# Performance work log

Measured on AMD Instinct MI355X. Metric: run time of the kernel, lower is better.

Reference implementation:

```python
import jax, jax.numpy as jnp
import numpy as np

N_GENES = 20000   # num_all_genes
D = 256           # embedding_dim
NNZ = 640000      # nonzeros in GO adjacency (~32 avg degree)
N_COND = 2000     # number of conditions
B = 16384         # batch size
MAXG = 5          # max_genes_per_condition
L = 2             # num_gnn_layers


def setup_inputs() -> dict:
    key = jax.random.key(0)
    ks = jax.random.split(key, 12)
    cond_idx = jax.random.randint(ks[0], (B,), 0, N_COND, dtype=jnp.int32)
    pert_embedding = jax.random.normal(ks[1], (N_GENES, D), jnp.float32) * 0.05
    gnn_kernels = jax.random.normal(ks[2], (L, D, D), jnp.float32) * 0.05
    mlp_w1 = jax.random.normal(ks[3], (D, D), jnp.float32) * 0.05
    mlp_b1 = jnp.zeros((D,), jnp.float32)
    mlp_w2 = jax.random.normal(ks[4], (D, D), jnp.float32) * 0.05
    mlp_b2 = jnp.zeros((D,), jnp.float32)
    adj_row = jax.random.randint(ks[5], (NNZ,), 0, N_GENES, dtype=jnp.int64)
    adj_col = jax.random.randint(ks[6], (NNZ,), 0, N_GENES, dtype=jnp.int64)
    adj_vals = jax.random.uniform(ks[7], (NNZ,), jnp.float32)
    cond_gene_idx = jax.random.randint(ks[8], (N_COND, MAXG), 0, N_GENES, dtype=jnp.int32)
    counts = jax.random.randint(ks[9], (N_COND,), 0, MAXG + 1)
    cond_gene_mask = (jnp.arange(MAXG)[None, :] < counts[:, None]).astype(jnp.float32)
    # padded slots get -1 index like the original (later clamped to 0)
    cond_gene_idx = jnp.where(cond_gene_mask > 0, cond_gene_idx, -1)
    return {
        'cond_idx': cond_idx,
        'pert_embedding': pert_embedding,
        'gnn_kernels': gnn_kernels,
        'mlp_w1': mlp_w1, 'mlp_b1': mlp_b1,
        'mlp_w2': mlp_w2, 'mlp_b2': mlp_b2,
        'adj_row': adj_row, 'adj_col': adj_col, 'adj_vals': adj_vals,
        'cond_gene_idx': cond_gene_idx, 'cond_gene_mask': cond_gene_mask,
    }


def reference(cond_idx, pert_embedding, gnn_kernels, mlp_w1, mlp_b1,
              mlp_w2, mlp_b2, adj_row, adj_col, adj_vals,
              cond_gene_idx, cond_gene_mask):
    # --- GNN over the full gene graph (sparse adjacency @ dense emb, then dense kernel) ---
    emb = pert_embedding  # [N, D]
    for i in range(L):
        # SpMM: aggregated[r] = sum_{nnz with row r} vals * emb[col]
        msgs = adj_vals[:, None] * emb[adj_col]            # [NNZ, D]
        agg = jax.ops.segment_sum(msgs, adj_row, num_segments=N_GENES)  # [N, D]
        emb = agg @ gnn_kernels[i]                          # [N, D]
        if i < L - 1:
            emb = jax.nn.relu(emb)

    # --- per-condition gather of up to MAXG gene embeddings, masked sum ---
    gidx = cond_gene_idx[cond_idx]          # [B, MAXG] int
    gmask = cond_gene_mask[cond_idx]        # [B, MAXG]
    gidx_safe = jnp.maximum(gidx, 0)
    gene_embs = emb[gidx_safe]              # [B, MAXG, D]
    summed = jnp.sum(gene_embs * gmask[:, :, None], axis=1)  # [B, D]
    n_genes = jnp.sum(gmask, axis=1)        # [B]

    # --- small MLP (applied when n_genes > 1), identity when ==1, zeros when ==0 ---
    h = jax.nn.relu(summed @ mlp_w1 + mlp_b1)
    mlp_out = jax.nn.relu(h @ mlp_w2 + mlp_b2)  # [B, D]

    n = n_genes[:, None]
    out = jnp.where(n == 0.0, 0.0, jnp.where(n == 1.0, summed, mlp_out))
    return out
```

## Files before the change

### kernel.cpp

```cpp
#include <hip/hip_runtime.h>

static constexpr int N_GENES = 20000;
static constexpr int D       = 256;
static constexpr int NNZ     = 640000;
static constexpr int BATCH   = 16384;
static constexpr int MAXG    = 5;
static constexpr int NR      = 8;
static constexpr int NB      = N_GENES * NR;
static constexpr int SCAN_BLKS = NB / 256;

using bf16x8 = __attribute__((ext_vector_type(8))) short;
using f32x4  = __attribute__((ext_vector_type(4))) float;

__device__ __forceinline__ unsigned short f2bf(float f) {
  unsigned int u = __builtin_bit_cast(unsigned int, f);
  u += 0x7fffu + ((u >> 16) & 1u);
  return (unsigned short)(u >> 16);
}
__device__ __forceinline__ float bf2f(unsigned short h) {
  unsigned int u = ((unsigned int)h) << 16;
  return __builtin_bit_cast(float, u);
}
__device__ __forceinline__ void gload16(const void* g, void* l) {
  __builtin_amdgcn_global_load_lds(
      (const __attribute__((address_space(1))) unsigned int*)g,
      (__attribute__((address_space(3))) unsigned int*)l, 16, 0, 0);
}
__device__ __forceinline__ unsigned colrange(int col) {
  return ((unsigned)col * 26215u) >> 26;
}

__global__ void count_buckets(const int* __restrict__ adj_row,
                              const int* __restrict__ adj_col, int* __restrict__ cnt) {
  int e = blockIdx.x * 256 + threadIdx.x;
  int r = adj_row[e];
  atomicAdd(&cnt[(r << 3) | colrange(adj_col[e])], 1);
}

__global__ __launch_bounds__(256)
void scan_partial(const int* __restrict__ cnt, int* __restrict__ bsum) {
  __shared__ int red[256];
  int b = blockIdx.x, t = threadIdx.x;
  red[t] = cnt[b * 256 + t];
  __syncthreads();
  for (int off = 128; off > 0; off >>= 1) {
    if (t < off) red[t] += red[t + off];
    __syncthreads();
  }
  if (t == 0) bsum[b] = red[0];
}

__global__ __launch_bounds__(1024)
void scan_mid(const int* __restrict__ bsum, int* __restrict__ bpre) {
  __shared__ int s[1024];
  int t = threadIdx.x;
  int x = (t < SCAN_BLKS) ? bsum[t] : 0;
  s[t] = x;
  __syncthreads();
  for (int off = 1; off < 1024; off <<= 1) {
    int v = (t >= off) ? s[t - off] : 0;
    __syncthreads();
    s[t] += v;
    __syncthreads();
  }
  if (t < SCAN_BLKS) bpre[t] = s[t] - x;
}

__global__ __launch_bounds__(256)
void scan_final(const int* __restrict__ cnt, const int* __restrict__ bpre,
                int* __restrict__ bptr, int* __restrict__ fill_ctr) {
  __shared__ int s[256];
  int b = blockIdx.x, t = threadIdx.x, i = b * 256 + t;
  int x = cnt[i];
  s[t] = x;
  __syncthreads();
  for (int off = 1; off < 256; off <<= 1) {
    int v = (t >= off) ? s[t - off] : 0;
    __syncthreads();
    s[t] += v;
    __syncthreads();
  }
  int e = bpre[b] + s[t] - x;
  bptr[i] = e;
  fill_ctr[i] = e;
  if (b == 0 && t == 0) bptr[NB] = NNZ;
}

__global__ __launch_bounds__(256)
void fused_fill_conv(const int* __restrict__ adj_row, const int* __restrict__ adj_col,
                     const float* __restrict__ vals, int* __restrict__ fill_ctr,
                     unsigned int* __restrict__ edges,
                     const float* __restrict__ gk, const float* __restrict__ w1,
                     const float* __restrict__ w2,
                     char* __restrict__ whi, char* __restrict__ wlo,
                     const float* __restrict__ pert, ushort4* __restrict__ pert_bf) {
  int b = blockIdx.x, t = threadIdx.x;
  if (b < 2500) {
    int e = b * 256 + t;
    int r = adj_row[e];
    int col = adj_col[e];
    int p = atomicAdd(&fill_ctr[(r << 3) | colrange(col)], 1);
    edges[p] = (unsigned int)col | ((unsigned int)f2bf(vals[e]) << 16);
  } else if (b < 2628) {
    int g = (b - 2500) * 256 + t;
    int wid = g >> 13, rest = g & 8191;
    const float* W = (wid == 0) ? gk : (wid == 1) ? gk + 65536 : (wid == 2) ? w1 : w2;
    int c  = rest >> 9;
    int nc = c >> 2, kt = c & 3;
    int o  = (rest & 511) << 4;
    int n  = o >> 7;
    int wb = (o & 127) ^ ((n & 7) << 4);
    int k  = wb >> 1;
    size_t obase = ((size_t)wid << 17) + ((size_t)c << 13) + o;
    unsigned short* ph = (unsigned short*)(whi + obase);
    unsigned short* pl = (unsigned short*)(wlo + obase);
    #pragma unroll
    for (int e2 = 0; e2 < 8; ++e2) {
      float f = W[(size_t)(kt * 64 + k + e2) * 256 + nc * 64 + n];
      unsigned short h = f2bf(f);
      ph[e2] = h;
      pl[e2] = f2bf(f - bf2f(h));
    }
  } else {
    int i = (b - 2628) * 256 + t;
    float4 v = reinterpret_cast<const float4*>(pert)[i];
    ushort4 r4;
    r4.x = f2bf(v.x); r4.y = f2bf(v.y); r4.z = f2bf(v.z); r4.w = f2bf(v.w);
    pert_bf[i] = r4;
  }
}

__global__ __launch_bounds__(256)
void spmm_csr_img(const int* __restrict__ bptr, const unsigned int* __restrict__ edges,
                  const unsigned short* __restrict__ src,
                  char* __restrict__ hi_img, char* __restrict__ lo_img) {
  int row = blockIdx.x * 4 + (threadIdx.x >> 6);
  int lane = threadIdx.x & 63;
  int beg = bptr[row << 3], end = bptr[(row << 3) + 8];
  const unsigned short* sp = src + lane * 4;
  float4 acc = {0.f, 0.f, 0.f, 0.f};
  int j = beg;
  for (; j + 8 <= end; j += 8) {
    unsigned int e0 = edges[j],     e1 = edges[j + 1], e2 = edges[j + 2], e3 = edges[j + 3];
    unsigned int e4 = edges[j + 4], e5 = edges[j + 5], e6 = edges[j + 6], e7 = edges[j + 7];
    ushort4 g0 = *reinterpret_cast<const ushort4*>(sp + (size_t)(e0 & 0xFFFFu) * D);
    ushort4 g1 = *reinterpret_cast<const ushort4*>(sp + (size_t)(e1 & 0xFFFFu) * D);
    ushort4 g2 = *reinterpret_cast<const ushort4*>(sp + (size_t)(e2 & 0xFFFFu) * D);
    ushort4 g3 = *reinterpret_cast<const ushort4*>(sp + (size_t)(e3 & 0xFFFFu) * D);
    ushort4 g4 = *reinterpret_cast<const ushort4*>(sp + (size_t)(e4 & 0xFFFFu) * D);
    ushort4 g5 = *reinterpret_cast<const ushort4*>(sp + (size_t)(e5 & 0xFFFFu) * D);
    ushort4 g6 = *reinterpret_cast<const ushort4*>(sp + (size_t)(e6 & 0xFFFFu) * D);
    ushort4 g7 = *reinterpret_cast<const ushort4*>(sp + (size_t)(e7 & 0xFFFFu) * D);
    float v0 = bf2f(e0 >> 16), v1 = bf2f(e1 >> 16), v2 = bf2f(e2 >> 16), v3 = bf2f(e3 >> 16);
    float v4 = bf2f(e4 >> 16), v5 = bf2f(e5 >> 16), v6 = bf2f(e6 >> 16), v7 = bf2f(e7 >> 16);
    acc.x += v0 * bf2f(g0.x); acc.y += v0 * bf2f(g0.y); acc.z += v0 * bf2f(g0.z); acc.w += v0 * bf2f(g0.w);
    acc.x += v1 * bf2f(g1.x); acc.y += v1 * bf2f(g1.y); acc.z += v1 * bf2f(g1.z); acc.w += v1 * bf2f(g1.w);
    acc.x += v2 * bf2f(g2.x); acc.y += v2 * bf2f(g2.y); acc.z += v2 * bf2f(g2.z); acc.w += v2 * bf2f(g2.w);
    acc.x += v3 * bf2f(g3.x); acc.y += v3 * bf2f(g3.y); acc.z += v3 * bf2f(g3.z); acc.w += v3 * bf2f(g3.w);
    acc.x += v4 * bf2f(g4.x); acc.y += v4 * bf2f(g4.y); acc.z += v4 * bf2f(g4.z); acc.w += v4 * bf2f(g4.w);
    acc.x += v5 * bf2f(g5.x); acc.y += v5 * bf2f(g5.y); acc.z += v5 * bf2f(g5.z); acc.w += v5 * bf2f(g5.w);
    acc.x += v6 * bf2f(g6.x); acc.y += v6 * bf2f(g6.y); acc.z += v6 * bf2f(g6.z); acc.w += v6 * bf2f(g6.w);
    acc.x += v7 * bf2f(g7.x); acc.y += v7 * bf2f(g7.y); acc.z += v7 * bf2f(g7.z); acc.w += v7 * bf2f(g7.w);
  }
  for (; j < end; ++j) {
    unsigned int e = edges[j];
    ushort4 g = *reinterpret_cast<const ushort4*>(sp + (size_t)(e & 0xFFFFu) * D);
    float v = bf2f(e >> 16);
    acc.x += v * bf2f(g.x); acc.y += v * bf2f(g.y); acc.z += v * bf2f(g.z); acc.w += v * bf2f(g.w);
  }
  int mt = row >> 7, r = row & 127, kt = lane >> 4;
  int wb = ((lane & 15) << 3) ^ ((r & 7) << 4);
  size_t off = ((size_t)(mt * 4 + kt) << 14) + (size_t)r * 128 + wb;
  float a4[4] = {acc.x, acc.y, acc.z, acc.w};
  ushort4 hi, lo;
  unsigned short* ph = (unsigned short*)&hi;
  unsigned short* pl = (unsigned short*)&lo;
  #pragma unroll
  for (int e = 0; e < 4; ++e) {
    unsigned short h = f2bf(a4[e]);
    ph[e] = h;
    pl[e] = f2bf(a4[e] - bf2f(h));
  }
  *reinterpret_cast<ushort4*>(hi_img + off) = hi;
  *reinterpret_cast<ushort4*>(lo_img + off) = lo;
}

__global__ __launch_bounds__(256)
void gather_conditions(const int* __restrict__ cond_idx, const int* __restrict__ cg_idx,
                       const float* __restrict__ cg_mask, const float* __restrict__ emb,
                       float* __restrict__ out, char* __restrict__ hi_img,
                       char* __restrict__ lo_img, float* __restrict__ ngenes) {
  int b = blockIdx.x * 4 + (threadIdx.x >> 6);
  int lane = threadIdx.x & 63;
  int c = cond_idx[b];
  float4 acc = {0.f, 0.f, 0.f, 0.f};
  float n = 0.f;
  #pragma unroll
  for (int g = 0; g < MAXG; ++g) {
    float m = cg_mask[c * MAXG + g];
    n += m;
    if (m > 0.f) {
      int gi = cg_idx[c * MAXG + g];
      float4 e = *reinterpret_cast<const float4*>(emb + (size_t)gi * D + lane * 4);
      acc.x += m * e.x; acc.y += m * e.y; acc.z += m * e.z; acc.w += m * e.w;
    }
  }
  *reinterpret_cast<float4*>(out + (size_t)b * D + lane * 4) = acc;
  int mt = b >> 7, r = b & 127, kt = lane >> 4;
  int wb = ((lane & 15) << 3) ^ ((r & 7) << 4);
  size_t off = ((size_t)(mt * 4 + kt) << 14) + (size_t)r * 128 + wb;
  float a4[4] = {acc.x, acc.y, acc.z, acc.w};
  ushort4 hi, lo;
  unsigned short* ph = (unsigned short*)&hi;
  unsigned short* pl = (unsigned short*)&lo;
  #pragma unroll
  for (int e = 0; e < 4; ++e) {
    unsigned short h = f2bf(a4[e]);
    ph[e] = h;
    pl[e] = f2bf(a4[e] - bf2f(h));
  }
  *reinterpret_cast<ushort4*>(hi_img + off) = hi;
  *reinterpret_cast<ushort4*>(lo_img + off) = lo;
  if (lane == 0) ngenes[b] = n;
}

__device__ __forceinline__ int xcd_swizzle(int orig, int nwg) {
  int xcd = orig & 7, boff = orig >> 3;
  int q = nwg >> 3, r8 = nwg & 7;
  return (xcd < r8 ? xcd * (q + 1) : r8 * (q + 1) + (xcd - r8) * q) + boff;
}

enum Epi { E_F32, E_RELU_BF16, E_HIMG, E_SELECT };

template <Epi EP>
__global__ __launch_bounds__(256)
void gemm_bf16x3(const char* __restrict__ Ahi, const char* __restrict__ Alo,
                 const char* __restrict__ Bhi, const char* __restrict__ Blo,
                 const float* __restrict__ bias, float* __restrict__ C,
                 unsigned short* __restrict__ Cbf,
                 char* __restrict__ Ohi, char* __restrict__ Olo,
                 const float* __restrict__ ngenes, int M) {
  __shared__ __align__(16) char smem[65536];
  char* sAh = smem;
  char* sAl = smem + 16384;
  char* sBh = smem + 32768;
  char* sBl = smem + 49152;

  const int t = threadIdx.x;
  const int w = t >> 6, l = t & 63;
  const int wr = w >> 1, wc = w & 1;
  const int wgid = xcd_swizzle(blockIdx.x, gridDim.x);
  const int mt = wgid >> 1, nt2 = wgid & 1;

  f32x4 acc[4][4] = {};
  const int rA = l & 15;
  const int kB = (l >> 4) << 4;
  const int xA = (rA & 7) << 4;

  for (int kt = 0; kt < 4; ++kt) {
    const char* gAh  = Ahi + ((size_t)(mt * 4 + kt) << 14);
    const char* gAl  = Alo + ((size_t)(mt * 4 + kt) << 14);
    const char* gBh0 = Bhi + ((size_t)((nt2 * 2 + 0) * 4 + kt) << 13);
    const char* gBl0 = Blo + ((size_t)((nt2 * 2 + 0) * 4 + kt) << 13);
    const char* gBh1 = Bhi + ((size_t)((nt2 * 2 + 1) * 4 + kt) << 13);
    const char* gBl1 = Blo + ((size_t)((nt2 * 2 + 1) * 4 + kt) << 13);
    #pragma unroll
    for (int j = 0; j < 4; ++j) {
      gload16(gAh + (j * 256 + t) * 16, sAh + j * 4096 + w * 1024);
      gload16(gAl + (j * 256 + t) * 16, sAl + j * 4096 + w * 1024);
    }
    #pragma unroll
    for (int j = 0; j < 2; ++j) {
      gload16(gBh0 + (j * 256 + t) * 16, sBh + j * 4096 + w * 1024);
      gload16(gBl0 + (j * 256 + t) * 16, sBl + j * 4096 + w * 1024);
      gload16(gBh1 + (j * 256 + t) * 16, sBh + 8192 + j * 4096 + w * 1024);
      gload16(gBl1 + (j * 256 + t) * 16, sBl + 8192 + j * 4096 + w * 1024);
    }
    asm volatile("s_waitcnt vmcnt(0)" ::: "memory");
    __syncthreads();
    #pragma unroll
    for (int ks = 0; ks < 2; ++ks) {
      bf16x8 ah[4], al[4], bh[4], bl[4];
      #pragma unroll
      for (int i = 0; i < 4; ++i) {
        int off = (wr * 64 + i * 16 + rA) * 128 + ((ks * 64 + kB) ^ xA);
        ah[i] = *(const bf16x8*)(sAh + off);
        al[i] = *(const bf16x8*)(sAl + off);
      }
      #pragma unroll
      for (int j = 0; j < 4; ++j) {
        int off = (wc * 64 + j * 16 + rA) * 128 + ((ks * 64 + kB) ^ xA);
        bh[j] = *(const bf16x8*)(sBh + off);
        bl[j] = *(const bf16x8*)(sBl + off);
      }
      #pragma unroll
      for (int i = 0; i < 4; ++i)
        #pragma unroll
        for (int j = 0; j < 4; ++j) {
          acc[i][j] = __builtin_amdgcn_mfma_f32_16x16x32_bf16(ah[i], bh[j], acc[i][j], 0, 0, 0);
          acc[i][j] = __builtin_amdgcn_mfma_f32_16x16x32_bf16(ah[i], bl[j], acc[i][j], 0, 0, 0);
          acc[i][j] = __builtin_amdgcn_mfma_f32_16x16x32_bf16(al[i], bh[j], acc[i][j], 0, 0, 0);
        }
    }
    __syncthreads();
  }

  const int cr = (l >> 4) << 2;
  const int cc = l & 15;
  #pragma unroll
  for (int i = 0; i < 4; ++i) {
    #pragma unroll
    for (int rr = 0; rr < 4; ++rr) {
      int rin  = wr * 64 + i * 16 + cr + rr;
      int grow = mt * 128 + rin;
      if (grow >= M) continue;
      bool wr_row = true;
      if (EP == E_SELECT) wr_row = (ngenes[grow] >= 1.5f);
      #pragma unroll
      for (int j = 0; j < 4; ++j) {
        float v   = acc[i][j][rr];
        int colin = wc * 64 + j * 16 + cc;
        int gcol  = nt2 * 128 + colin;
        if (EP == E_HIMG || EP == E_SELECT) v += bias[gcol];
        if (EP != E_F32) v = fmaxf(v, 0.f);
        if (EP == E_HIMG) {
          int kt2 = nt2 * 2 + (colin >> 6);
          int k2  = colin & 63;
          int wb  = (k2 << 1) ^ ((rin & 7) << 4);
          size_t off = ((size_t)(mt * 4 + kt2) << 14) + (size_t)rin * 128 + wb;
          unsigned short h16 = f2bf(v);
          *(unsigned short*)(Ohi + off) = h16;
          *(unsigned short*)(Olo + off) = f2bf(v - bf2f(h16));
        } else if (EP == E_RELU_BF16) {
          Cbf[(size_t)grow * 256 + gcol] = f2bf(v);
        } else if (wr_row) {
          C[(size_t)grow * 256 + gcol] = v;
        }
      }
    }
  }
}

extern "C" void kernel_launch(void* const* d_in, const int* in_sizes, int n_in,
                              void* d_out, int out_size, void* d_ws, size_t ws_size,
                              hipStream_t stream) {
  const int*   cond_idx = (const int*)d_in[0];
  const float* pert     = (const float*)d_in[1];
  const float* gnn_k    = (const float*)d_in[2];
  const float* w1       = (const float*)d_in[3];
  const float* b1       = (const float*)d_in[4];
  const float* w2       = (const float*)d_in[5];
  const float* b2       = (const float*)d_in[6];
  const int*   adj_row  = (const int*)d_in[7];
  const int*   adj_col  = (const int*)d_in[8];
  const float* adj_vals = (const float*)d_in[9];
  const int*   cg_idx   = (const int*)d_in[10];
  const float* cg_mask  = (const float*)d_in[11];
  float* out = (float*)d_out;

  char* w = (char*)d_ws;
  auto alloc = [&](size_t bytes) {
    void* p = w;
    w += (bytes + 255) & ~size_t(255);
    return p;
  };
  constexpr int MT_G = (N_GENES + 127) / 128;
  constexpr int MT_B = BATCH / 128;
  char*         aggHi   = (char*)alloc((size_t)MT_G * 4 * 16384);
  char*         aggLo   = (char*)alloc((size_t)MT_G * 4 * 16384);
  float*        embf    = (float*)alloc((size_t)N_GENES * D * 4);
  char*         sumHi   = (char*)alloc((size_t)MT_B * 4 * 16384);
  char*         sumLo   = (char*)alloc((size_t)MT_B * 4 * 16384);
  char*         hHi     = (char*)alloc((size_t)MT_B * 4 * 16384);
  char*         hLo     = (char*)alloc((size_t)MT_B * 4 * 16384);
  char*         wHi     = (char*)alloc((size_t)4 << 17);
  char*         wLo     = (char*)alloc((size_t)4 << 17);
  unsigned int* edges   = (unsigned int*)alloc((size_t)NNZ * 4);
  int*          cnt     = (int*)alloc((size_t)NB * 4);
  int*          bptr    = (int*)alloc((size_t)(NB + 4) * 4);
  int*          fill_ctr= (int*)alloc((size_t)NB * 4);
  int*          bsum    = (int*)alloc((size_t)1024 * 4);
  int*          bpre    = (int*)alloc((size_t)1024 * 4);
  float*        ngenes  = (float*)alloc((size_t)BATCH * 4);

  unsigned short* pert_bf = (unsigned short*)sumHi;
  unsigned short* embf_bf = (unsigned short*)embf;

  hipMemsetAsync(cnt, 0, (size_t)NB * 4, stream);
  count_buckets<<<NNZ / 256, 256, 0, stream>>>(adj_row, adj_col, cnt);
  scan_partial<<<SCAN_BLKS, 256, 0, stream>>>(cnt, bsum);
  scan_mid<<<1, 1024, 0, stream>>>(bsum, bpre);
  scan_final<<<SCAN_BLKS, 256, 0, stream>>>(cnt, bpre, bptr, fill_ctr);
  fused_fill_conv<<<2500 + 128 + 5000, 256, 0, stream>>>(
      adj_row, adj_col, adj_vals, fill_ctr, edges,
      gnn_k, w1, w2, wHi, wLo, pert, (ushort4*)pert_bf);

  spmm_csr_img<<<N_GENES / 4, 256, 0, stream>>>(bptr, edges, pert_bf, aggHi, aggLo);
  gemm_bf16x3<E_RELU_BF16><<<2 * MT_G, 256, 0, stream>>>(
      aggHi, aggLo, wHi, wLo, nullptr, nullptr, embf_bf, nullptr, nullptr, nullptr, N_GENES);

  spmm_csr_img<<<N_GENES / 4, 256, 0, stream>>>(bptr, edges, embf_bf, aggHi, aggLo);
  gemm_bf16x3<E_F32><<<2 * MT_G, 256, 0, stream>>>(
      aggHi, aggLo, wHi + (1 << 17), wLo + (1 << 17), nullptr, embf, nullptr, nullptr, nullptr, nullptr, N_GENES);

  gather_conditions<<<BATCH / 4, 256, 0, stream>>>(cond_idx, cg_idx, cg_mask, embf,
                                                   out, sumHi, sumLo, ngenes);

  gemm_bf16x3<E_HIMG><<<2 * MT_B, 256, 0, stream>>>(
      sumHi, sumLo, wHi + (2 << 17), wLo + (2 << 17), b1, nullptr, nullptr, hHi, hLo, nullptr, BATCH);

  gemm_bf16x3<E_SELECT><<<2 * MT_B, 256, 0, stream>>>(
      hHi, hLo, wHi + (3 << 17), wLo + (3 << 17), b2, out, nullptr, nullptr, nullptr, ngenes, BATCH);
}
```

Baseline: 313.2 us.

## Fuse CSR build preprocessing into one cooperative kernel with grid syncs

Replaces the memset, bucket count, three scan kernels and the fill/convert kernel with a single cooperative kernel of 640 blocks that uses grid-wide syncs between phases. The middle scan is folded into each block summing the preceding block totals. The aim is to remove several kernel launch gaps and a memset. The cost is grid-sync overhead, a redundant O(blocks) prefix sum per block, and lower parallelism for the atomic phases since they now run as grid-stride loops.

```diff
diff --git a/kernel.cpp b/kernel.cpp
--- a/kernel.cpp
+++ b/kernel.cpp
@@ -1,4 +1,7 @@
 #include <hip/hip_runtime.h>
+#include <hip/hip_cooperative_groups.h>
+
+namespace cg = cooperative_groups;
 
 static constexpr int N_GENES = 20000;
 static constexpr int D       = 256;
@@ -8,6 +11,8 @@
 static constexpr int NR      = 8;
 static constexpr int NB      = N_GENES * NR;
 static constexpr int SCAN_BLKS = NB / 256;
+static constexpr int COOP_BLOCKS = 640;
+static constexpr int COOP_TH  = COOP_BLOCKS * 256;
 
 using bf16x8 = __attribute__((ext_vector_type(8))) short;
 using f32x4  = __attribute__((ext_vector_type(4))) float;
@@ -30,80 +35,24 @@
   return ((unsigned)col * 26215u) >> 26;
 }
 
-__global__ void count_buckets(const int* __restrict__ adj_row,
-                              const int* __restrict__ adj_col, int* __restrict__ cnt) {
-  int e = blockIdx.x * 256 + threadIdx.x;
-  int r = adj_row[e];
-  atomicAdd(&cnt[(r << 3) | colrange(adj_col[e])], 1);
-}
-
 __global__ __launch_bounds__(256)
-void scan_partial(const int* __restrict__ cnt, int* __restrict__ bsum) {
-  __shared__ int red[256];
-  int b = blockIdx.x, t = threadIdx.x;
-  red[t] = cnt[b * 256 + t];
-  __syncthreads();
-  for (int off = 128; off > 0; off >>= 1) {
-    if (t < off) red[t] += red[t + off];
-    __syncthreads();
-  }
-  if (t == 0) bsum[b] = red[0];
-}
-
-__global__ __launch_bounds__(1024)
-void scan_mid(const int* __restrict__ bsum, int* __restrict__ bpre) {
-  __shared__ int s[1024];
-  int t = threadIdx.x;
-  int x = (t < SCAN_BLKS) ? bsum[t] : 0;
-  s[t] = x;
-  __syncthreads();
-  for (int off = 1; off < 1024; off <<= 1) {
-    int v = (t >= off) ? s[t - off] : 0;
-    __syncthreads();
-    s[t] += v;
-    __syncthreads();
-  }
-  if (t < SCAN_BLKS) bpre[t] = s[t] - x;
-}
-
-__global__ __launch_bounds__(256)
-void scan_final(const int* __restrict__ cnt, const int* __restrict__ bpre,
-                int* __restrict__ bptr, int* __restrict__ fill_ctr) {
+void build_all(const int* __restrict__ adj_row, const int* __restrict__ adj_col,
+               const float* __restrict__ vals,
+               const float* __restrict__ gk, const float* __restrict__ w1,
+               const float* __restrict__ w2,
+               int* __restrict__ cnt, int* __restrict__ fill_ctr,
+               int* __restrict__ bptr, int* __restrict__ bsum,
+               unsigned int* __restrict__ edges,
+               char* __restrict__ whi, char* __restrict__ wlo,
+               const float* __restrict__ pert, ushort4* __restrict__ pert_bf) {
+  cg::grid_group grid = cg::this_grid();
   __shared__ int s[256];
-  int b = blockIdx.x, t = threadIdx.x, i = b * 256 + t;
-  int x = cnt[i];
-  s[t] = x;
-  __syncthreads();
-  for (int off = 1; off < 256; off <<= 1) {
-    int v = (t >= off) ? s[t - off] : 0;
-    __syncthreads();
-    s[t] += v;
-    __syncthreads();
-  }
-  int e = bpre[b] + s[t] - x;
-  bptr[i] = e;
-  fill_ctr[i] = e;
-  if (b == 0 && t == 0) bptr[NB] = NNZ;
-}
-
-__global__ __launch_bounds__(256)
-void fused_fill_conv(const int* __restrict__ adj_row, const int* __restrict__ adj_col,
-                     const float* __restrict__ vals, int* __restrict__ fill_ctr,
-                     unsigned int* __restrict__ edges,
-                     const float* __restrict__ gk, const float* __restrict__ w1,
-                     const float* __restrict__ w2,
-                     char* __restrict__ whi, char* __restrict__ wlo,
-                     const float* __restrict__ pert, ushort4* __restrict__ pert_bf) {
-  int b = blockIdx.x, t = threadIdx.x;
-  if (b < 2500) {
-    int e = b * 256 + t;
-    int r = adj_row[e];
-    int col = adj_col[e];
-    int p = atomicAdd(&fill_ctr[(r << 3) | colrange(col)], 1);
-    edges[p] = (unsigned int)col | ((unsigned int)f2bf(vals[e]) << 16);
-  } else if (b < 2628) {
-    int g = (b - 2500) * 256 + t;
-    int wid = g >> 13, rest = g & 8191;
+  const int b = blockIdx.x, t = threadIdx.x;
+  const int gid = b * 256 + t;
+
+  if (gid < NB) cnt[gid] = 0;
+  if (gid < 32768) {
+    int wid = gid >> 13, rest = gid & 8191;
     const float* W = (wid == 0) ? gk : (wid == 1) ? gk + 65536 : (wid == 2) ? w1 : w2;
     int c  = rest >> 9;
     int nc = c >> 2, kt = c & 3;
@@ -121,12 +70,62 @@
       ph[e2] = h;
       pl[e2] = f2bf(f - bf2f(h));
     }
-  } else {
-    int i = (b - 2628) * 256 + t;
+  }
+  for (int i = gid; i < N_GENES * D / 4; i += COOP_TH) {
     float4 v = reinterpret_cast<const float4*>(pert)[i];
     ushort4 r4;
     r4.x = f2bf(v.x); r4.y = f2bf(v.y); r4.z = f2bf(v.z); r4.w = f2bf(v.w);
     pert_bf[i] = r4;
+  }
+  grid.sync();
+
+  for (int e = gid; e < NNZ; e += COOP_TH)
+    atomicAdd(&cnt[(adj_row[e] << 3) | colrange(adj_col[e])], 1);
+  grid.sync();
+
+  if (b < SCAN_BLKS) {
+    s[t] = cnt[b * 256 + t];
+    __syncthreads();
+    for (int off = 128; off > 0; off >>= 1) {
+      if (t < off) s[t] += s[t + off];
+      __syncthreads();
+    }
+    if (t == 0) bsum[b] = s[0];
+  }
+  grid.sync();
+
+  if (b < SCAN_BLKS) {
+    int part = 0;
+    for (int c = t; c < b; c += 256) part += bsum[c];
+    s[t] = part;
+    __syncthreads();
+    for (int off = 128; off > 0; off >>= 1) {
+      if (t < off) s[t] += s[t + off];
+      __syncthreads();
+    }
+    int bpre = s[0];
+    __syncthreads();
+    int i = b * 256 + t;
+    int x = cnt[i];
+    s[t] = x;
+    __syncthreads();
+    for (int off = 1; off < 256; off <<= 1) {
+      int v = (t >= off) ? s[t - off] : 0;
+      __syncthreads();
+      s[t] += v;
+      __syncthreads();
+    }
+    int e = bpre + s[t] - x;
+    bptr[i] = e;
+    fill_ctr[i] = e;
+    if (b == 0 && t == 0) bptr[NB] = NNZ;
+  }
+  grid.sync();
+
+  for (int e = gid; e < NNZ; e += COOP_TH) {
+    int col = adj_col[e];
+    int p = atomicAdd(&fill_ctr[(adj_row[e] << 3) | colrange(col)], 1);
+    edges[p] = (unsigned int)col | ((unsigned int)f2bf(vals[e]) << 16);
   }
 }
 
@@ -380,20 +379,20 @@
   int*          bptr    = (int*)alloc((size_t)(NB + 4) * 4);
   int*          fill_ctr= (int*)alloc((size_t)NB * 4);
   int*          bsum    = (int*)alloc((size_t)1024 * 4);
-  int*          bpre    = (int*)alloc((size_t)1024 * 4);
   float*        ngenes  = (float*)alloc((size_t)BATCH * 4);
 
   unsigned short* pert_bf = (unsigned short*)sumHi;
   unsigned short* embf_bf = (unsigned short*)embf;
 
-  hipMemsetAsync(cnt, 0, (size_t)NB * 4, stream);
-  count_buckets<<<NNZ / 256, 256, 0, stream>>>(adj_row, adj_col, cnt);
-  scan_partial<<<SCAN_BLKS, 256, 0, stream>>>(cnt, bsum);
-  scan_mid<<<1, 1024, 0, stream>>>(bsum, bpre);
-  scan_final<<<SCAN_BLKS, 256, 0, stream>>>(cnt, bpre, bptr, fill_ctr);
-  fused_fill_conv<<<2500 + 128 + 5000, 256, 0, stream>>>(
-      adj_row, adj_col, adj_vals, fill_ctr, edges,
-      gnn_k, w1, w2, wHi, wLo, pert, (ushort4*)pert_bf);
+  ushort4* pert_bf_v = (ushort4*)pert_bf;
+  void* args[] = {
+      (void*)&adj_row, (void*)&adj_col, (void*)&adj_vals,
+      (void*)&gnn_k, (void*)&w1, (void*)&w2,
+      (void*)&cnt, (void*)&fill_ctr, (void*)&bptr, (void*)&bsum,
+      (void*)&edges, (void*)&wHi, (void*)&wLo,
+      (void*)&pert, (void*)&pert_bf_v};
+  hipLaunchCooperativeKernel((void*)build_all, dim3(COOP_BLOCKS), dim3(256),
+                             args, 0, stream);
 
   spmm_csr_img<<<N_GENES / 4, 256, 0, stream>>>(bptr, edges, pert_bf, aggHi, aggLo);
   gemm_bf16x3<E_RELU_BF16><<<2 * MT_G, 256, 0, stream>>>(
```

Result: slower. 614.2 us (+96.1%).
